# Performance work log

Hardware: AMD Instinct MI355X
Metric: run time of the kernel (lower is better)

## Reference

```python
import jax, jax.numpy as jnp
import numpy as np
from jax import lax


def setup_inputs() -> dict:
    key = jax.random.key(0)
    ks = jax.random.split(key, 6)
    T, B, I, H, K = 128, 64, 1024, 1024, 8
    s = 1.0 / np.sqrt(H)  # PyTorch LSTM init scale
    return {
        "x": jax.random.normal(ks[0], (T, B, I), dtype=jnp.float32),
        "coef": jax.random.uniform(ks[1], (T, K), dtype=jnp.float32),
        "w_ih": jax.random.uniform(ks[2], (K, 4 * H, I), dtype=jnp.float32, minval=-s, maxval=s),
        "w_hh": jax.random.uniform(ks[3], (K, 4 * H, H), dtype=jnp.float32, minval=-s, maxval=s),
        "b_ih": jax.random.uniform(ks[4], (K, 4 * H), dtype=jnp.float32, minval=-s, maxval=s),
        "b_hh": jax.random.uniform(ks[5], (K, 4 * H), dtype=jnp.float32, minval=-s, maxval=s),
        "h0": jnp.zeros((B, H), dtype=jnp.float32),
        "c0": jnp.zeros((B, H), dtype=jnp.float32),
    }


def reference(x, coef, w_ih, w_hh, b_ih, b_hh, h0, c0):
    # x: [T, B, I]; coef: [T, K]; w_ih: [K, 4H, I]; w_hh: [K, 4H, H]
    H = h0.shape[-1]
    cw = jax.nn.softmax(coef, axis=1)  # [T, K] mixture weights per timestep

    def step(carry, inp):
        h, c = carry            # [B, H], [B, H]
        xt, ct = inp            # [B, I], [K]
        # Synthesize this timestep's LSTM weights (mixture over k meta models)
        Wih = jnp.einsum('k,kgi->gi', ct, w_ih)   # [4H, I]
        Whh = jnp.einsum('k,kgh->gh', ct, w_hh)   # [4H, H]
        b = ct @ b_ih + ct @ b_hh                 # [4H]
        gates = xt @ Wih.T + h @ Whh.T + b        # [B, 4H]
        i, f, g, o = jnp.split(gates, 4, axis=-1)  # PyTorch gate order i,f,g,o
        i, f, o = jax.nn.sigmoid(i), jax.nn.sigmoid(f), jax.nn.sigmoid(o)
        g = jnp.tanh(g)
        c_new = f * c + i * g
        h_new = o * jnp.tanh(c_new)
        return (h_new, c_new), h_new

    (_, _), ys = lax.scan(step, (h0, c0), (x, cw))
    return ys  # [T, B, H] concatenated per-step outputs
```

## Files before the change

### kernel.cpp

```cpp
#include <hip/hip_runtime.h>
#include <math.h>
#include <stdint.h>

#define TT 128
#define BB 64
#define II 1024
#define HH 1024
#define KK 8
#define G4 4096
#define MM 8192
#define TCH 32
#define NCH (TT / TCH)

typedef _Float16 f16x8 __attribute__((ext_vector_type(8)));
typedef float    f32x4 __attribute__((ext_vector_type(4)));

#define OFF_CW    0
#define OFF_BIAS  4096
#define OFF_C     2101248
#define OFF_H0    2363392
#define OFF_H1    2494464
#define OFF_GX    2625536
#define OFF_WIH   69734400
#define OFF_X8    203952128
#define OFF_WCH   OFF_WIH
#define WS_REQ    338169856

__global__ __launch_bounds__(256) void softmax_bias_kernel(
    const float* __restrict__ coef,
    const float* __restrict__ b_ih,
    const float* __restrict__ b_hh,
    float* __restrict__ ws)
{
    int t = blockIdx.x;
    float c[KK];
    float m = -1e30f;
    #pragma unroll
    for (int k = 0; k < KK; ++k) { c[k] = coef[t*KK + k]; m = fmaxf(m, c[k]); }
    float s = 0.f;
    #pragma unroll
    for (int k = 0; k < KK; ++k) { c[k] = expf(c[k] - m); s += c[k]; }
    float inv = 1.f / s;
    #pragma unroll
    for (int k = 0; k < KK; ++k) c[k] *= inv;
    if (threadIdx.x < KK) ws[t*KK + threadIdx.x] = c[threadIdx.x];
    float* bias = ws + 1024;
    for (int g = threadIdx.x; g < G4; g += blockDim.x) {
        float acc = 0.f;
        #pragma unroll
        for (int k = 0; k < KK; ++k)
            acc += c[k] * (b_ih[k*G4 + g] + b_hh[k*G4 + g]);
        bias[t*G4 + g] = acc;
    }
}

__global__ __launch_bounds__(256) void conv_f16_kernel(
    const float* __restrict__ src, _Float16* __restrict__ dst, long n8)
{
    long v = (long)blockIdx.x * 256 + threadIdx.x;
    if (v >= n8) return;
    const float* s = src + v * 8;
    f16x8 o;
    #pragma unroll
    for (int e = 0; e < 8; ++e) o[e] = (_Float16)s[e];
    *(f16x8*)(dst + v * 8) = o;
}

__global__ __launch_bounds__(256) void mix_chunk_kernel(
    const float* __restrict__ w_hh,
    const float* __restrict__ cw,
    _Float16* __restrict__ wchunk,
    int t0)
{
    __shared__ float cws[TCH * KK];
    const int tid = threadIdx.x;
    if (tid < TCH * KK) cws[tid] = cw[t0 * KK + tid];

    long v = (long)blockIdx.x * 256 + tid;
    const int l  = (int)(v & 63);
    const int kk = (int)((v >> 6) & 31);
    const int bj = (int)(v >> 11);
    const int q  = l & 15;
    const int grow = (q >> 2) * HH + bj * 4 + (q & 3);
    const int col  = kk * 32 + 8 * (l >> 4);

    float w8[KK][8];
    #pragma unroll
    for (int k = 0; k < KK; ++k) {
        const float* s = w_hh + ((size_t)k * G4 + grow) * II + col;
        #pragma unroll
        for (int e = 0; e < 8; ++e) w8[k][e] = s[e];
    }
    __syncthreads();

    const size_t slot = ((size_t)bj * 32 + kk) * 64 + l;
    #pragma unroll 4
    for (int tt = 0; tt < TCH; ++tt) {
        float acc[8] = {0,0,0,0,0,0,0,0};
        #pragma unroll
        for (int k = 0; k < KK; ++k) {
            float c = cws[tt * KK + k];
            #pragma unroll
            for (int e = 0; e < 8; ++e) acc[e] += c * w8[k][e];
        }
        f16x8 o;
        #pragma unroll
        for (int e = 0; e < 8; ++e) o[e] = (_Float16)acc[e];
        *(f16x8*)(wchunk + ((size_t)tt << 22) + slot * 8) = o;
    }
}

__global__ __launch_bounds__(256) void x8_kernel(
    const float* __restrict__ x, const float* __restrict__ cw,
    _Float16* __restrict__ x8)
{
    long v = (long)blockIdx.x * 256 + threadIdx.x;
    if (v >= (long)KK * MM * (II/8)) return;
    int k   = (int)(v / (MM * (II/8)));
    long rem = v % (MM * (II/8));
    int row = (int)(rem / (II/8));
    int i8  = (int)(rem % (II/8));
    int t   = row >> 6;
    float sc = cw[t*KK + k];
    const float* s = x + (long)row * II + i8 * 8;
    f16x8 o;
    #pragma unroll
    for (int e = 0; e < 8; ++e) o[e] = (_Float16)(sc * s[e]);
    *(f16x8*)(x8 + v * 8) = o;
}

__global__ __launch_bounds__(256) void hinit_kernel(
    const float* __restrict__ h0, _Float16* __restrict__ hws)
{
    int idx = blockIdx.x * 256 + threadIdx.x;
    hws[idx] = (_Float16)h0[idx];
}

#define PAD 80
__global__ __launch_bounds__(256) void phaseA_gemm(
    const _Float16* __restrict__ x8,
    const _Float16* __restrict__ wih,
    _Float16* __restrict__ gx)
{
    __shared__ _Float16 As[128][PAD];
    __shared__ _Float16 Bs[128][PAD];
    const int tid  = threadIdx.x;
    const int lane = tid & 63;
    const int wv   = tid >> 6;
    const int wr   = wv >> 1, wc = wv & 1;
    const int bm   = blockIdx.x & 63;
    const int bn   = blockIdx.x >> 6;
    const size_t m0 = (size_t)bm * 128, n0 = (size_t)bn * 128;

    f32x4 acc[4][4];
    #pragma unroll
    for (int i = 0; i < 4; ++i)
        #pragma unroll
        for (int j = 0; j < 4; ++j) acc[i][j] = (f32x4){0.f,0.f,0.f,0.f};

    const int srow = tid >> 3;
    const int scol = (tid & 7) * 8;

    for (int kt = 0; kt < 128; ++kt) {
        const int kseg = kt >> 4;
        const int i0   = (kt & 15) * 64;
        const size_t abase = (size_t)kseg * MM * II + i0;
        const size_t bbase = (size_t)kseg * G4 * II + i0;
        #pragma unroll
        for (int it = 0; it < 4; ++it) {
            int r = it * 32 + srow;
            *(f16x8*)&As[r][scol] = *(const f16x8*)(x8 + abase + (m0 + r) * II + scol);
            *(f16x8*)&Bs[r][scol] = *(const f16x8*)(wih + bbase + (n0 + r) * II + scol);
        }
        __syncthreads();
        #pragma unroll
        for (int half = 0; half < 2; ++half) {
            const int kc = half * 32 + 8 * (lane >> 4);
            f16x8 a[4], b[4];
            #pragma unroll
            for (int mf = 0; mf < 4; ++mf)
                a[mf] = *(const f16x8*)&As[wr*64 + mf*16 + (lane & 15)][kc];
            #pragma unroll
            for (int nf = 0; nf < 4; ++nf)
                b[nf] = *(const f16x8*)&Bs[wc*64 + nf*16 + (lane & 15)][kc];
            #pragma unroll
            for (int mf = 0; mf < 4; ++mf)
                #pragma unroll
                for (int nf = 0; nf < 4; ++nf)
                    acc[mf][nf] = __builtin_amdgcn_mfma_f32_16x16x32_f16(
                        a[mf], b[nf], acc[mf][nf], 0, 0, 0);
        }
        __syncthreads();
    }
    #pragma unroll
    for (int mf = 0; mf < 4; ++mf)
        #pragma unroll
        for (int nf = 0; nf < 4; ++nf) {
            size_t col = n0 + wc*64 + nf*16 + (lane & 15);
            size_t rw  = m0 + wr*64 + mf*16 + 4*(lane >> 4);
            #pragma unroll
            for (int r = 0; r < 4; ++r)
                gx[(rw + r) * G4 + col] = (_Float16)acc[mf][nf][r];
        }
}

__global__ __launch_bounds__(512) void stepB5_kernel(
    const _Float16* __restrict__ wmix_t,
    const _Float16* __restrict__ gx_t,
    const float* __restrict__ bias_t,
    const _Float16* __restrict__ hin,
    _Float16* __restrict__ hout,
    float* __restrict__ cst,
    float* __restrict__ out_t)
{
    __shared__ float gpart[8][BB][17];

    const int tid  = threadIdx.x;
    const int lane = tid & 63;
    const int wv   = tid >> 6;
    const int bj   = blockIdx.x;
    const int j0   = bj * 4;
    const int q    = lane & 15;
    const int kch  = 8 * (lane >> 4);

    float pre_gx[4], pre_bias[4], pre_c = 0.f;
    const int eb  = tid & 63;
    const int ejj = tid >> 6;
    if (tid < 256) {
        #pragma unroll
        for (int gate = 0; gate < 4; ++gate) {
            pre_gx[gate]   = (float)gx_t[(size_t)eb * G4 + gate * HH + j0 + ejj];
            pre_bias[gate] = bias_t[gate * HH + j0 + ejj];
        }
        pre_c = cst[(size_t)eb * HH + j0 + ejj];
    }

    const _Float16* w0 = wmix_t + (((size_t)bj * 32 + 4 * wv) * 64) * 8;
    f16x8 pb[4];
    #pragma unroll
    for (int u = 0; u < 4; ++u)
        pb[u] = *(const f16x8*)(w0 + ((size_t)u * 64 + lane) * 8);

    f32x4 acc[4];
    #pragma unroll
    for (int mf = 0; mf < 4; ++mf) acc[mf] = (f32x4){0.f,0.f,0.f,0.f};

    #pragma unroll
    for (int u = 0; u < 4; ++u) {
        const int kk = 4 * wv + u;
        const int hp = kk * 32 + kch;
        f16x8 a[4];
        #pragma unroll
        for (int mf = 0; mf < 4; ++mf)
            a[mf] = *(const f16x8*)(hin + (size_t)(mf * 16 + q) * HH + hp);
        #pragma unroll
        for (int mf = 0; mf < 4; ++mf)
            acc[mf] = __builtin_amdgcn_mfma_f32_16x16x32_f16(a[mf], pb[u], acc[mf], 0, 0, 0);
    }

    #pragma unroll
    for (int mf = 0; mf < 4; ++mf) {
        #pragma unroll
        for (int r = 0; r < 4; ++r) {
            int m = mf * 16 + 4 * (lane >> 4) + r;
            gpart[wv][m][q] = acc[mf][r];
        }
    }
    __syncthreads();

    if (tid < 256) {
        const int j = j0 + ejj;
        float gval[4];
        #pragma unroll
        for (int gate = 0; gate < 4; ++gate) {
            int qq = gate * 4 + ejj;
            float v = 0.f;
            #pragma unroll
            for (int w = 0; w < 8; ++w) v += gpart[w][eb][qq];
            gval[gate] = v + pre_gx[gate] + pre_bias[gate];
        }
        float iv = 1.f / (1.f + expf(-gval[0]));
        float fv = 1.f / (1.f + expf(-gval[1]));
        float gv = tanhf(gval[2]);
        float ov = 1.f / (1.f + expf(-gval[3]));
        float c  = fv * pre_c + iv * gv;
        cst[(size_t)eb * HH + j] = c;
        float h  = ov * tanhf(c);
        out_t[(size_t)eb * HH + j] = h;
        hout[(size_t)eb * HH + j] = (_Float16)h;
    }
}

#define TI 128
__global__ __launch_bounds__(256) void step_kernel(
    const float* __restrict__ x_t, const float* __restrict__ hprev,
    const float* __restrict__ cprev, const float* __restrict__ w_ih,
    const float* __restrict__ w_hh, const float* __restrict__ cw_t,
    const float* __restrict__ bias_t, float* __restrict__ cstate,
    float* __restrict__ out_t)
{
    __shared__ float xh_s[BB][TI + 1];
    __shared__ float w_s[16][TI + 1];
    __shared__ float gex[4 * BB * 4];
    const int tid = threadIdx.x;
    const int j0 = blockIdx.x * 4;
    const int b = tid & 63;
    const int gate = tid >> 6;
    float cw[KK];
    #pragma unroll
    for (int k = 0; k < KK; ++k) cw[k] = cw_t[k];
    float acc[4] = {0.f, 0.f, 0.f, 0.f};
    for (int ci = 0; ci < II + HH; ci += TI) {
        for (int e = tid; e < BB * TI; e += 256) {
            int bb = e >> 7, cc = e & (TI - 1);
            int c = ci + cc;
            xh_s[bb][cc] = (c < II) ? x_t[bb * II + c] : hprev[bb * HH + (c - II)];
        }
        const float* wbase = (ci < II) ? w_ih : w_hh;
        const int cbase = (ci < II) ? ci : (ci - II);
        for (int e = tid; e < 16 * TI; e += 256) {
            int r = e >> 7, cc = e & (TI - 1);
            int grw = (r >> 2) * HH + j0 + (r & 3);
            size_t off = (size_t)grw * II + (size_t)(cbase + cc);
            float wm = 0.f;
            #pragma unroll
            for (int k = 0; k < KK; ++k)
                wm += cw[k] * wbase[(size_t)k * ((size_t)G4 * II) + off];
            w_s[r][cc] = wm;
        }
        __syncthreads();
        for (int c = 0; c < TI; ++c) {
            float xv = xh_s[b][c];
            #pragma unroll
            for (int d = 0; d < 4; ++d)
                acc[d] += xv * w_s[(gate << 2) + d][c];
        }
        __syncthreads();
    }
    #pragma unroll
    for (int d = 0; d < 4; ++d) {
        acc[d] += bias_t[gate * HH + j0 + d];
        gex[gate * 256 + b * 4 + d] = acc[d];
    }
    __syncthreads();
    const int b2 = tid & 63, d2 = tid >> 6;
    float iv = gex[0 * 256 + b2 * 4 + d2];
    float fv = gex[1 * 256 + b2 * 4 + d2];
    float gv = gex[2 * 256 + b2 * 4 + d2];
    float ov = gex[3 * 256 + b2 * 4 + d2];
    float si = 1.f / (1.f + expf(-iv));
    float sf = 1.f / (1.f + expf(-fv));
    float so = 1.f / (1.f + expf(-ov));
    float tg = tanhf(gv);
    int j = j0 + d2;
    float cold = cprev[b2 * HH + j];
    float cnew = sf * cold + si * tg;
    cstate[b2 * HH + j] = cnew;
    out_t[b2 * HH + j] = so * tanhf(cnew);
}

extern "C" void kernel_launch(void* const* d_in, const int* in_sizes, int n_in,
                              void* d_out, int out_size, void* d_ws, size_t ws_size,
                              hipStream_t stream) {
    const float* x    = (const float*)d_in[0];
    const float* coef = (const float*)d_in[1];
    const float* w_ih = (const float*)d_in[2];
    const float* w_hh = (const float*)d_in[3];
    const float* b_ih = (const float*)d_in[4];
    const float* b_hh = (const float*)d_in[5];
    const float* h0   = (const float*)d_in[6];
    const float* c0   = (const float*)d_in[7];
    float* out = (float*)d_out;
    char* ws   = (char*)d_ws;
    float* cw_f   = (float*)(ws + OFF_CW);
    float* bias_f = (float*)(ws + OFF_BIAS);
    float* c_f    = (float*)(ws + OFF_C);

    softmax_bias_kernel<<<TT, 256, 0, stream>>>(coef, b_ih, b_hh, (float*)ws);

    if (ws_size >= (size_t)WS_REQ) {
        _Float16* h0p  = (_Float16*)(ws + OFF_H0);
        _Float16* h1p  = (_Float16*)(ws + OFF_H1);
        _Float16* gx   = (_Float16*)(ws + OFF_GX);
        _Float16* wihf = (_Float16*)(ws + OFF_WIH);
        _Float16* x8   = (_Float16*)(ws + OFF_X8);
        _Float16* wch  = (_Float16*)(ws + OFF_WCH);

        conv_f16_kernel<<<16384, 256, 0, stream>>>(w_ih, wihf, (long)KK*G4*II/8);
        x8_kernel<<<32768, 256, 0, stream>>>(x, cw_f, x8);
        hinit_kernel<<<256, 256, 0, stream>>>(h0, h0p);
        hipMemcpyAsync(c_f, c0, (size_t)BB*HH*4, hipMemcpyDeviceToDevice, stream);

        phaseA_gemm<<<2048, 256, 0, stream>>>(x8, wihf, gx);

        for (int ch = 0; ch < NCH; ++ch) {
            const int t0 = ch * TCH;
            mix_chunk_kernel<<<2048, 256, 0, stream>>>(w_hh, cw_f, wch, t0);
            for (int tt = 0; tt < TCH; ++tt) {
                const int t = t0 + tt;
                stepB5_kernel<<<256, 512, 0, stream>>>(
                    wch + ((size_t)tt << 22),
                    gx + (size_t)t * BB * G4,
                    bias_f + (size_t)t * G4,
                    (t & 1) ? h1p : h0p,
                    (t & 1) ? h0p : h1p,
                    c_f,
                    out + (size_t)t * BB * HH);
            }
        }
    } else {
        for (int t = 0; t < TT; ++t) {
            const float* xt    = x + (size_t)t * BB * II;
            const float* hprev = (t == 0) ? h0 : out + (size_t)(t - 1) * BB * HH;
            const float* cprev = (t == 0) ? c0 : c_f;
            step_kernel<<<HH / 4, 256, 0, stream>>>(
                xt, hprev, cprev, w_ih, w_hh,
                cw_f + (size_t)t * KK,
                bias_f + (size_t)t * G4,
                c_f,
                out + (size_t)t * BB * HH);
        }
    }
}
```

Measured before the change: 2.360 ms.

## Replace input-projection mega-GEMM with per-timestep mixed-weight GEMMs

Instead of scaling x by each mixture coefficient and running one large GEMM with a reduction over K*I, this mixes w_ih into per-timestep f16 weights in chunks and runs a small 64x4096x1024 MFMA GEMM per timestep. That cuts input-projection FLOPs by about a factor of K and drops the x8 and w_ih conversion passes. In exchange it adds heavy memory traffic to write and re-read a mixed weight matrix for every timestep. The chunk size drops to 16, which doubles the number of mix launches for both w_ih and w_hh.

```diff
diff --git a/kernel.cpp b/kernel.cpp
--- a/kernel.cpp
+++ b/kernel.cpp
@@ -9,7 +9,7 @@
 #define KK 8
 #define G4 4096
 #define MM 8192
-#define TCH 32
+#define TCH 16
 #define NCH (TT / TCH)
 
 typedef _Float16 f16x8 __attribute__((ext_vector_type(8)));
@@ -21,9 +21,8 @@
 #define OFF_H0    2363392
 #define OFF_H1    2494464
 #define OFF_GX    2625536
-#define OFF_WIH   69734400
-#define OFF_X8    203952128
-#define OFF_WCH   OFF_WIH
+#define OFF_XF    69734400
+#define OFF_WCH   86511616
 #define WS_REQ    338169856
 
 __global__ __launch_bounds__(256) void softmax_bias_kernel(
@@ -67,7 +66,7 @@
 }
 
 __global__ __launch_bounds__(256) void mix_chunk_kernel(
-    const float* __restrict__ w_hh,
+    const float* __restrict__ wsrc,
     const float* __restrict__ cw,
     _Float16* __restrict__ wchunk,
     int t0)
@@ -87,7 +86,7 @@
     float w8[KK][8];
     #pragma unroll
     for (int k = 0; k < KK; ++k) {
-        const float* s = w_hh + ((size_t)k * G4 + grow) * II + col;
+        const float* s = wsrc + ((size_t)k * G4 + grow) * II + col;
         #pragma unroll
         for (int e = 0; e < 8; ++e) w8[k][e] = s[e];
     }
@@ -110,25 +109,6 @@
     }
 }
 
-__global__ __launch_bounds__(256) void x8_kernel(
-    const float* __restrict__ x, const float* __restrict__ cw,
-    _Float16* __restrict__ x8)
-{
-    long v = (long)blockIdx.x * 256 + threadIdx.x;
-    if (v >= (long)KK * MM * (II/8)) return;
-    int k   = (int)(v / (MM * (II/8)));
-    long rem = v % (MM * (II/8));
-    int row = (int)(rem / (II/8));
-    int i8  = (int)(rem % (II/8));
-    int t   = row >> 6;
-    float sc = cw[t*KK + k];
-    const float* s = x + (long)row * II + i8 * 8;
-    f16x8 o;
-    #pragma unroll
-    for (int e = 0; e < 8; ++e) o[e] = (_Float16)(sc * s[e]);
-    *(f16x8*)(x8 + v * 8) = o;
-}
-
 __global__ __launch_bounds__(256) void hinit_kernel(
     const float* __restrict__ h0, _Float16* __restrict__ hws)
 {
@@ -136,72 +116,74 @@
     hws[idx] = (_Float16)h0[idx];
 }
 
-#define PAD 80
-__global__ __launch_bounds__(256) void phaseA_gemm(
-    const _Float16* __restrict__ x8,
-    const _Float16* __restrict__ wih,
-    _Float16* __restrict__ gx)
-{
-    __shared__ _Float16 As[128][PAD];
-    __shared__ _Float16 Bs[128][PAD];
+__global__ __launch_bounds__(512) void gxA_kernel(
+    const _Float16* __restrict__ xf,
+    const _Float16* __restrict__ wch,
+    _Float16* __restrict__ gx,
+    int t0)
+{
+    __shared__ float gpart[8][BB][17];
+
     const int tid  = threadIdx.x;
     const int lane = tid & 63;
     const int wv   = tid >> 6;
-    const int wr   = wv >> 1, wc = wv & 1;
-    const int bm   = blockIdx.x & 63;
-    const int bn   = blockIdx.x >> 6;
-    const size_t m0 = (size_t)bm * 128, n0 = (size_t)bn * 128;
-
-    f32x4 acc[4][4];
-    #pragma unroll
-    for (int i = 0; i < 4; ++i)
-        #pragma unroll
-        for (int j = 0; j < 4; ++j) acc[i][j] = (f32x4){0.f,0.f,0.f,0.f};
-
-    const int srow = tid >> 3;
-    const int scol = (tid & 7) * 8;
-
-    for (int kt = 0; kt < 128; ++kt) {
-        const int kseg = kt >> 4;
-        const int i0   = (kt & 15) * 64;
-        const size_t abase = (size_t)kseg * MM * II + i0;
-        const size_t bbase = (size_t)kseg * G4 * II + i0;
-        #pragma unroll
-        for (int it = 0; it < 4; ++it) {
-            int r = it * 32 + srow;
-            *(f16x8*)&As[r][scol] = *(const f16x8*)(x8 + abase + (m0 + r) * II + scol);
-            *(f16x8*)&Bs[r][scol] = *(const f16x8*)(wih + bbase + (n0 + r) * II + scol);
-        }
-        __syncthreads();
-        #pragma unroll
-        for (int half = 0; half < 2; ++half) {
-            const int kc = half * 32 + 8 * (lane >> 4);
-            f16x8 a[4], b[4];
+    const int bj   = blockIdx.x & 255;
+    const int tt   = blockIdx.x >> 8;
+    const int t    = t0 + tt;
+    const int j0   = bj * 4;
+    const int q    = lane & 15;
+    const int kch  = 8 * (lane >> 4);
+
+    const _Float16* xf_t = xf + (size_t)t * BB * II;
+    _Float16*       gx_t = gx + (size_t)t * BB * G4;
+
+    const _Float16* w0 = wch + ((size_t)tt << 22)
+                             + (((size_t)bj * 32 + 4 * wv) * 64) * 8;
+    f16x8 pb[4];
+    #pragma unroll
+    for (int u = 0; u < 4; ++u)
+        pb[u] = *(const f16x8*)(w0 + ((size_t)u * 64 + lane) * 8);
+
+    f32x4 acc[4];
+    #pragma unroll
+    for (int mf = 0; mf < 4; ++mf) acc[mf] = (f32x4){0.f,0.f,0.f,0.f};
+
+    #pragma unroll
+    for (int u = 0; u < 4; ++u) {
+        const int kk = 4 * wv + u;
+        const int hp = kk * 32 + kch;
+        f16x8 a[4];
+        #pragma unroll
+        for (int mf = 0; mf < 4; ++mf)
+            a[mf] = *(const f16x8*)(xf_t + (size_t)(mf * 16 + q) * II + hp);
+        #pragma unroll
+        for (int mf = 0; mf < 4; ++mf)
+            acc[mf] = __builtin_amdgcn_mfma_f32_16x16x32_f16(a[mf], pb[u], acc[mf], 0, 0, 0);
+    }
+
+    #pragma unroll
+    for (int mf = 0; mf < 4; ++mf) {
+        #pragma unroll
+        for (int r = 0; r < 4; ++r) {
+            int m = mf * 16 + 4 * (lane >> 4) + r;
+            gpart[wv][m][q] = acc[mf][r];
+        }
+    }
+    __syncthreads();
+
+    if (tid < 256) {
+        const int b  = tid & 63;
+        const int jj = tid >> 6;
+        const int j  = j0 + jj;
+        #pragma unroll
+        for (int gate = 0; gate < 4; ++gate) {
+            int qq = gate * 4 + jj;
+            float v = 0.f;
             #pragma unroll
-            for (int mf = 0; mf < 4; ++mf)
-                a[mf] = *(const f16x8*)&As[wr*64 + mf*16 + (lane & 15)][kc];
-            #pragma unroll
-            for (int nf = 0; nf < 4; ++nf)
-                b[nf] = *(const f16x8*)&Bs[wc*64 + nf*16 + (lane & 15)][kc];
-            #pragma unroll
-            for (int mf = 0; mf < 4; ++mf)
-                #pragma unroll
-                for (int nf = 0; nf < 4; ++nf)
-                    acc[mf][nf] = __builtin_amdgcn_mfma_f32_16x16x32_f16(
-                        a[mf], b[nf], acc[mf][nf], 0, 0, 0);
-        }
-        __syncthreads();
-    }
-    #pragma unroll
-    for (int mf = 0; mf < 4; ++mf)
-        #pragma unroll
-        for (int nf = 0; nf < 4; ++nf) {
-            size_t col = n0 + wc*64 + nf*16 + (lane & 15);
-            size_t rw  = m0 + wr*64 + mf*16 + 4*(lane >> 4);
-            #pragma unroll
-            for (int r = 0; r < 4; ++r)
-                gx[(rw + r) * G4 + col] = (_Float16)acc[mf][nf][r];
-        }
+            for (int w = 0; w < 8; ++w) v += gpart[w][b][qq];
+            gx_t[(size_t)b * G4 + gate * HH + j] = (_Float16)v;
+        }
+    }
 }
 
 __global__ __launch_bounds__(512) void stepB5_kernel(
@@ -379,19 +361,21 @@
     softmax_bias_kernel<<<TT, 256, 0, stream>>>(coef, b_ih, b_hh, (float*)ws);
 
     if (ws_size >= (size_t)WS_REQ) {
-        _Float16* h0p  = (_Float16*)(ws + OFF_H0);
-        _Float16* h1p  = (_Float16*)(ws + OFF_H1);
-        _Float16* gx   = (_Float16*)(ws + OFF_GX);
-        _Float16* wihf = (_Float16*)(ws + OFF_WIH);
-        _Float16* x8   = (_Float16*)(ws + OFF_X8);
-        _Float16* wch  = (_Float16*)(ws + OFF_WCH);
-
-        conv_f16_kernel<<<16384, 256, 0, stream>>>(w_ih, wihf, (long)KK*G4*II/8);
-        x8_kernel<<<32768, 256, 0, stream>>>(x, cw_f, x8);
+        _Float16* h0p = (_Float16*)(ws + OFF_H0);
+        _Float16* h1p = (_Float16*)(ws + OFF_H1);
+        _Float16* gx  = (_Float16*)(ws + OFF_GX);
+        _Float16* xf  = (_Float16*)(ws + OFF_XF);
+        _Float16* wch = (_Float16*)(ws + OFF_WCH);
+
+        conv_f16_kernel<<<4096, 256, 0, stream>>>(x, xf, (long)MM * II / 8);
         hinit_kernel<<<256, 256, 0, stream>>>(h0, h0p);
         hipMemcpyAsync(c_f, c0, (size_t)BB*HH*4, hipMemcpyDeviceToDevice, stream);
 
-        phaseA_gemm<<<2048, 256, 0, stream>>>(x8, wihf, gx);
+        for (int ch = 0; ch < NCH; ++ch) {
+            const int t0 = ch * TCH;
+            mix_chunk_kernel<<<2048, 256, 0, stream>>>(w_ih, cw_f, wch, t0);
+            gxA_kernel<<<TCH * 256, 512, 0, stream>>>(xf, wch, gx, t0);
+        }
 
         for (int ch = 0; ch < NCH; ++ch) {
             const int t0 = ch * TCH;
```

Result: slower. 2.807 ms (+18.9%).

## Fold mixture coefficients into input GEMM epilogue instead of replicating scaled x

Applied to the files above, without the earlier changes.

Removes the kernel that materialized eight coefficient-scaled fp16 copies of x. The GEMM now reads a single fp16 copy of x and accumulates each meta-model segment into a partial accumulator, which is scaled by that timestep's coefficient and added to a total. This drops a large intermediate buffer write and read, at the cost of doubling the accumulator registers, which may reduce occupancy.

```diff
diff --git a/kernel.cpp b/kernel.cpp
--- a/kernel.cpp
+++ b/kernel.cpp
@@ -22,7 +22,7 @@
 #define OFF_H1    2494464
 #define OFF_GX    2625536
 #define OFF_WIH   69734400
-#define OFF_X8    203952128
+#define OFF_XF    203952128
 #define OFF_WCH   OFF_WIH
 #define WS_REQ    338169856
 
@@ -110,25 +110,6 @@
     }
 }
 
-__global__ __launch_bounds__(256) void x8_kernel(
-    const float* __restrict__ x, const float* __restrict__ cw,
-    _Float16* __restrict__ x8)
-{
-    long v = (long)blockIdx.x * 256 + threadIdx.x;
-    if (v >= (long)KK * MM * (II/8)) return;
-    int k   = (int)(v / (MM * (II/8)));
-    long rem = v % (MM * (II/8));
-    int row = (int)(rem / (II/8));
-    int i8  = (int)(rem % (II/8));
-    int t   = row >> 6;
-    float sc = cw[t*KK + k];
-    const float* s = x + (long)row * II + i8 * 8;
-    f16x8 o;
-    #pragma unroll
-    for (int e = 0; e < 8; ++e) o[e] = (_Float16)(sc * s[e]);
-    *(f16x8*)(x8 + v * 8) = o;
-}
-
 __global__ __launch_bounds__(256) void hinit_kernel(
     const float* __restrict__ h0, _Float16* __restrict__ hws)
 {
@@ -137,9 +118,10 @@
 }
 
 #define PAD 80
-__global__ __launch_bounds__(256) void phaseA_gemm(
-    const _Float16* __restrict__ x8,
+__global__ __launch_bounds__(256) void phaseA2_gemm(
+    const _Float16* __restrict__ xf,
     const _Float16* __restrict__ wih,
+    const float* __restrict__ cw,
     _Float16* __restrict__ gx)
 {
     __shared__ _Float16 As[128][PAD];
@@ -152,11 +134,19 @@
     const int bn   = blockIdx.x >> 6;
     const size_t m0 = (size_t)bm * 128, n0 = (size_t)bn * 128;
 
-    f32x4 acc[4][4];
+    const int t_wave = bm * 2 + wr;
+    float sc[KK];
+    #pragma unroll
+    for (int k = 0; k < KK; ++k) sc[k] = cw[t_wave * KK + k];
+
+    f32x4 accT[4][4], accP[4][4];
     #pragma unroll
     for (int i = 0; i < 4; ++i)
         #pragma unroll
-        for (int j = 0; j < 4; ++j) acc[i][j] = (f32x4){0.f,0.f,0.f,0.f};
+        for (int j = 0; j < 4; ++j) {
+            accT[i][j] = (f32x4){0.f,0.f,0.f,0.f};
+            accP[i][j] = (f32x4){0.f,0.f,0.f,0.f};
+        }
 
     const int srow = tid >> 3;
     const int scol = (tid & 7) * 8;
@@ -164,12 +154,11 @@
     for (int kt = 0; kt < 128; ++kt) {
         const int kseg = kt >> 4;
         const int i0   = (kt & 15) * 64;
-        const size_t abase = (size_t)kseg * MM * II + i0;
         const size_t bbase = (size_t)kseg * G4 * II + i0;
         #pragma unroll
         for (int it = 0; it < 4; ++it) {
             int r = it * 32 + srow;
-            *(f16x8*)&As[r][scol] = *(const f16x8*)(x8 + abase + (m0 + r) * II + scol);
+            *(f16x8*)&As[r][scol] = *(const f16x8*)(xf + (m0 + r) * II + i0 + scol);
             *(f16x8*)&Bs[r][scol] = *(const f16x8*)(wih + bbase + (n0 + r) * II + scol);
         }
         __syncthreads();
@@ -187,10 +176,22 @@
             for (int mf = 0; mf < 4; ++mf)
                 #pragma unroll
                 for (int nf = 0; nf < 4; ++nf)
-                    acc[mf][nf] = __builtin_amdgcn_mfma_f32_16x16x32_f16(
-                        a[mf], b[nf], acc[mf][nf], 0, 0, 0);
+                    accP[mf][nf] = __builtin_amdgcn_mfma_f32_16x16x32_f16(
+                        a[mf], b[nf], accP[mf][nf], 0, 0, 0);
         }
         __syncthreads();
+        if ((kt & 15) == 15) {
+            const float s = sc[kseg];
+            #pragma unroll
+            for (int mf = 0; mf < 4; ++mf)
+                #pragma unroll
+                for (int nf = 0; nf < 4; ++nf) {
+                    #pragma unroll
+                    for (int r = 0; r < 4; ++r)
+                        accT[mf][nf][r] += s * accP[mf][nf][r];
+                    accP[mf][nf] = (f32x4){0.f,0.f,0.f,0.f};
+                }
+        }
     }
     #pragma unroll
     for (int mf = 0; mf < 4; ++mf)
@@ -200,7 +201,7 @@
             size_t rw  = m0 + wr*64 + mf*16 + 4*(lane >> 4);
             #pragma unroll
             for (int r = 0; r < 4; ++r)
-                gx[(rw + r) * G4 + col] = (_Float16)acc[mf][nf][r];
+                gx[(rw + r) * G4 + col] = (_Float16)accT[mf][nf][r];
         }
 }
 
@@ -383,15 +384,15 @@
         _Float16* h1p  = (_Float16*)(ws + OFF_H1);
         _Float16* gx   = (_Float16*)(ws + OFF_GX);
         _Float16* wihf = (_Float16*)(ws + OFF_WIH);
-        _Float16* x8   = (_Float16*)(ws + OFF_X8);
+        _Float16* xf   = (_Float16*)(ws + OFF_XF);
         _Float16* wch  = (_Float16*)(ws + OFF_WCH);
 
         conv_f16_kernel<<<16384, 256, 0, stream>>>(w_ih, wihf, (long)KK*G4*II/8);
-        x8_kernel<<<32768, 256, 0, stream>>>(x, cw_f, x8);
+        conv_f16_kernel<<<4096, 256, 0, stream>>>(x, xf, (long)MM*II/8);
         hinit_kernel<<<256, 256, 0, stream>>>(h0, h0p);
         hipMemcpyAsync(c_f, c0, (size_t)BB*HH*4, hipMemcpyDeviceToDevice, stream);
 
-        phaseA_gemm<<<2048, 256, 0, stream>>>(x8, wihf, gx);
+        phaseA2_gemm<<<2048, 256, 0, stream>>>(xf, wihf, cw_f, gx);
 
         for (int ch = 0; ch < NCH; ++ch) {
             const int t0 = ch * TCH;
```

New measurement: 2.288 ms. -3.0%, faster.

## Rewrite input-projection GEMM with 256x256 tiles, async LDS loads and double buffering

Applied to the files above, without the earlier changes.

Replaces the 128x128 phase-A GEMM, which used synchronous register-staged loads, with a 256x256-tile, 512-thread kernel. The new kernel uses global_load_lds direct-to-LDS copies into double buffers with an XOR swizzle, fine-grained vmcnt waits, and s_setprio around MFMA bursts so loads for the next K tiles overlap compute. The aim is to hide memory latency and raise operand reuse in the large x·W_ih GEMM. The cost is heavy register pressure from 32 accumulators per lane, fewer blocks, and fragile hand-counted waitcnt ordering.

```diff
diff --git a/kernel.cpp b/kernel.cpp
--- a/kernel.cpp
+++ b/kernel.cpp
@@ -11,6 +11,7 @@
 #define MM 8192
 #define TCH 32
 #define NCH (TT / TCH)
+#define NT 128
 
 typedef _Float16 f16x8 __attribute__((ext_vector_type(8)));
 typedef float    f32x4 __attribute__((ext_vector_type(4)));
@@ -26,6 +27,10 @@
 #define OFF_WCH   OFF_WIH
 #define WS_REQ    338169856
 
+#define BARRIER() do { asm volatile("" ::: "memory"); \
+                       __builtin_amdgcn_s_barrier();  \
+                       asm volatile("" ::: "memory"); } while (0)
+
 __global__ __launch_bounds__(256) void softmax_bias_kernel(
     const float* __restrict__ coef,
     const float* __restrict__ b_ih,
@@ -64,50 +69,6 @@
     #pragma unroll
     for (int e = 0; e < 8; ++e) o[e] = (_Float16)s[e];
     *(f16x8*)(dst + v * 8) = o;
-}
-
-__global__ __launch_bounds__(256) void mix_chunk_kernel(
-    const float* __restrict__ w_hh,
-    const float* __restrict__ cw,
-    _Float16* __restrict__ wchunk,
-    int t0)
-{
-    __shared__ float cws[TCH * KK];
-    const int tid = threadIdx.x;
-    if (tid < TCH * KK) cws[tid] = cw[t0 * KK + tid];
-
-    long v = (long)blockIdx.x * 256 + tid;
-    const int l  = (int)(v & 63);
-    const int kk = (int)((v >> 6) & 31);
-    const int bj = (int)(v >> 11);
-    const int q  = l & 15;
-    const int grow = (q >> 2) * HH + bj * 4 + (q & 3);
-    const int col  = kk * 32 + 8 * (l >> 4);
-
-    float w8[KK][8];
-    #pragma unroll
-    for (int k = 0; k < KK; ++k) {
-        const float* s = w_hh + ((size_t)k * G4 + grow) * II + col;
-        #pragma unroll
-        for (int e = 0; e < 8; ++e) w8[k][e] = s[e];
-    }
-    __syncthreads();
-
-    const size_t slot = ((size_t)bj * 32 + kk) * 64 + l;
-    #pragma unroll 4
-    for (int tt = 0; tt < TCH; ++tt) {
-        float acc[8] = {0,0,0,0,0,0,0,0};
-        #pragma unroll
-        for (int k = 0; k < KK; ++k) {
-            float c = cws[tt * KK + k];
-            #pragma unroll
-            for (int e = 0; e < 8; ++e) acc[e] += c * w8[k][e];
-        }
-        f16x8 o;
-        #pragma unroll
-        for (int e = 0; e < 8; ++e) o[e] = (_Float16)acc[e];
-        *(f16x8*)(wchunk + ((size_t)tt << 22) + slot * 8) = o;
-    }
 }
 
 __global__ __launch_bounds__(256) void x8_kernel(
@@ -129,6 +90,50 @@
     *(f16x8*)(x8 + v * 8) = o;
 }
 
+__global__ __launch_bounds__(256) void mix_chunk_kernel(
+    const float* __restrict__ w_hh,
+    const float* __restrict__ cw,
+    _Float16* __restrict__ wchunk,
+    int t0)
+{
+    __shared__ float cws[TCH * KK];
+    const int tid = threadIdx.x;
+    if (tid < TCH * KK) cws[tid] = cw[t0 * KK + tid];
+
+    long v = (long)blockIdx.x * 256 + tid;
+    const int l  = (int)(v & 63);
+    const int kk = (int)((v >> 6) & 31);
+    const int bj = (int)(v >> 11);
+    const int q  = l & 15;
+    const int grow = (q >> 2) * HH + bj * 4 + (q & 3);
+    const int col  = kk * 32 + 8 * (l >> 4);
+
+    float w8[KK][8];
+    #pragma unroll
+    for (int k = 0; k < KK; ++k) {
+        const float* s = w_hh + ((size_t)k * G4 + grow) * II + col;
+        #pragma unroll
+        for (int e = 0; e < 8; ++e) w8[k][e] = s[e];
+    }
+    __syncthreads();
+
+    const size_t slot = ((size_t)bj * 32 + kk) * 64 + l;
+    #pragma unroll 4
+    for (int tt = 0; tt < TCH; ++tt) {
+        float acc[8] = {0,0,0,0,0,0,0,0};
+        #pragma unroll
+        for (int k = 0; k < KK; ++k) {
+            float c = cws[tt * KK + k];
+            #pragma unroll
+            for (int e = 0; e < 8; ++e) acc[e] += c * w8[k][e];
+        }
+        f16x8 o;
+        #pragma unroll
+        for (int e = 0; e < 8; ++e) o[e] = (_Float16)acc[e];
+        *(f16x8*)(wchunk + ((size_t)tt << 22) + slot * 8) = o;
+    }
+}
+
 __global__ __launch_bounds__(256) void hinit_kernel(
     const float* __restrict__ h0, _Float16* __restrict__ hws)
 {
@@ -136,68 +141,151 @@
     hws[idx] = (_Float16)h0[idx];
 }
 
-#define PAD 80
-__global__ __launch_bounds__(256) void phaseA_gemm(
+__device__ __forceinline__ int swz(int b) {
+    return b ^ (((b >> 9) & 1) << 5) ^ (((b >> 10) & 1) << 4);
+}
+
+__global__ __launch_bounds__(512) void phaseA3_gemm(
     const _Float16* __restrict__ x8,
     const _Float16* __restrict__ wih,
     _Float16* __restrict__ gx)
 {
-    __shared__ _Float16 As[128][PAD];
-    __shared__ _Float16 Bs[128][PAD];
+    __shared__ _Float16 ldsA[2 * 16384];
+    __shared__ _Float16 ldsB[2 * 16384];
+
     const int tid  = threadIdx.x;
     const int lane = tid & 63;
     const int wv   = tid >> 6;
-    const int wr   = wv >> 1, wc = wv & 1;
-    const int bm   = blockIdx.x & 63;
-    const int bn   = blockIdx.x >> 6;
-    const size_t m0 = (size_t)bm * 128, n0 = (size_t)bn * 128;
-
-    f32x4 acc[4][4];
-    #pragma unroll
-    for (int i = 0; i < 4; ++i)
+    const int wm   = wv >> 2;
+    const int wn   = wv & 3;
+    const int bm   = blockIdx.x & 31;
+    const int bn   = blockIdx.x >> 5;
+    const size_t m0 = (size_t)bm * 256, n0 = (size_t)bn * 256;
+
+    int srow[4], scol[4], pl2[4];
+    #pragma unroll
+    for (int j = 0; j < 4; ++j) {
+        int p = j * 8192 + tid * 16;
+        int L = swz(p);
+        srow[j] = L >> 7;
+        scol[j] = (L & 127) >> 1;
+        pl2[j]  = p >> 1;
+    }
+
+    auto stA = [&](int j, int tk) {
+        const int kseg = tk >> 4, i0v = (tk & 15) * 64;
+        const _Float16* s = x8 + (size_t)kseg * MM * II
+                               + (m0 + srow[j]) * II + i0v + scol[j];
+        __builtin_amdgcn_global_load_lds(s, &ldsA[(tk & 1) * 16384 + pl2[j]], 16, 0, 0);
+    };
+    auto stB = [&](int j, int tk) {
+        const int kseg = tk >> 4, i0v = (tk & 15) * 64;
+        const _Float16* s = wih + (size_t)kseg * G4 * II
+                               + (n0 + srow[j]) * II + i0v + scol[j];
+        __builtin_amdgcn_global_load_lds(s, &ldsB[(tk & 1) * 16384 + pl2[j]], 16, 0, 0);
+    };
+
+    const int baseA = (wm * 128 + (lane & 15)) * 128 + (lane >> 4) * 16;
+    const int baseB = (wn * 64  + (lane & 15)) * 128 + (lane >> 4) * 16;
+
+    auto rdA = [&](int buf, int mf, int ks) -> f16x8 {
+        int q = baseA + mf * 2048 + ks * 64;
+        return *(const f16x8*)((const char*)&ldsA[buf * 16384] + swz(q));
+    };
+    auto rdB = [&](int buf, int nf, int ks) -> f16x8 {
+        int q = baseB + nf * 2048 + ks * 64;
+        return *(const f16x8*)((const char*)&ldsB[buf * 16384] + swz(q));
+    };
+
+    f32x4 acc[8][4];
+    #pragma unroll
+    for (int i = 0; i < 8; ++i)
         #pragma unroll
         for (int j = 0; j < 4; ++j) acc[i][j] = (f32x4){0.f,0.f,0.f,0.f};
 
-    const int srow = tid >> 3;
-    const int scol = (tid & 7) * 8;
-
-    for (int kt = 0; kt < 128; ++kt) {
-        const int kseg = kt >> 4;
-        const int i0   = (kt & 15) * 64;
-        const size_t abase = (size_t)kseg * MM * II + i0;
-        const size_t bbase = (size_t)kseg * G4 * II + i0;
-        #pragma unroll
-        for (int it = 0; it < 4; ++it) {
-            int r = it * 32 + srow;
-            *(f16x8*)&As[r][scol] = *(const f16x8*)(x8 + abase + (m0 + r) * II + scol);
-            *(f16x8*)&Bs[r][scol] = *(const f16x8*)(wih + bbase + (n0 + r) * II + scol);
-        }
-        __syncthreads();
-        #pragma unroll
-        for (int half = 0; half < 2; ++half) {
-            const int kc = half * 32 + 8 * (lane >> 4);
-            f16x8 a[4], b[4];
-            #pragma unroll
-            for (int mf = 0; mf < 4; ++mf)
-                a[mf] = *(const f16x8*)&As[wr*64 + mf*16 + (lane & 15)][kc];
-            #pragma unroll
-            for (int nf = 0; nf < 4; ++nf)
-                b[nf] = *(const f16x8*)&Bs[wc*64 + nf*16 + (lane & 15)][kc];
-            #pragma unroll
-            for (int mf = 0; mf < 4; ++mf)
-                #pragma unroll
-                for (int nf = 0; nf < 4; ++nf)
-                    acc[mf][nf] = __builtin_amdgcn_mfma_f32_16x16x32_f16(
-                        a[mf], b[nf], acc[mf][nf], 0, 0, 0);
-        }
-        __syncthreads();
-    }
-    #pragma unroll
-    for (int mf = 0; mf < 4; ++mf)
+    stA(0,0); stA(2,0);
+    stB(0,0); stB(1,0);
+    stB(2,0); stB(3,0);
+    stA(1,0); stA(3,0);
+    stA(0,1); stA(2,1);
+    stB(0,1); stB(1,1);
+    stB(2,1); stB(3,1);
+
+    for (int kt = 0; kt < NT; ++kt) {
+        const int buf = kt & 1;
+        if (kt < NT - 1) { asm volatile("s_waitcnt vmcnt(8)" ::: "memory"); }
+        else             { asm volatile("s_waitcnt vmcnt(2)" ::: "memory"); }
+        BARRIER();
+        if (kt + 1 < NT) { stA(1, kt + 1); stA(3, kt + 1); }
+        f16x8 a0[4][2], b[4][2];
+        #pragma unroll
+        for (int mf = 0; mf < 4; ++mf) {
+            a0[mf][0] = rdA(buf, mf, 0);
+            a0[mf][1] = rdA(buf, mf, 1);
+        }
         #pragma unroll
         for (int nf = 0; nf < 4; ++nf) {
-            size_t col = n0 + wc*64 + nf*16 + (lane & 15);
-            size_t rw  = m0 + wr*64 + mf*16 + 4*(lane >> 4);
+            b[nf][0] = rdB(buf, nf, 0);
+            b[nf][1] = rdB(buf, nf, 1);
+        }
+        __builtin_amdgcn_s_setprio(1);
+        #pragma unroll
+        for (int mf = 0; mf < 4; ++mf)
+            #pragma unroll
+            for (int nf = 0; nf < 2; ++nf) {
+                acc[mf][nf] = __builtin_amdgcn_mfma_f32_16x16x32_f16(a0[mf][0], b[nf][0], acc[mf][nf], 0, 0, 0);
+                acc[mf][nf] = __builtin_amdgcn_mfma_f32_16x16x32_f16(a0[mf][1], b[nf][1], acc[mf][nf], 0, 0, 0);
+            }
+        __builtin_amdgcn_s_setprio(0);
+        BARRIER();
+        if (kt + 2 < NT) { stA(0, kt + 2); stA(2, kt + 2); }
+        __builtin_amdgcn_s_setprio(1);
+        #pragma unroll
+        for (int mf = 0; mf < 4; ++mf)
+            #pragma unroll
+            for (int nf = 2; nf < 4; ++nf) {
+                acc[mf][nf] = __builtin_amdgcn_mfma_f32_16x16x32_f16(a0[mf][0], b[nf][0], acc[mf][nf], 0, 0, 0);
+                acc[mf][nf] = __builtin_amdgcn_mfma_f32_16x16x32_f16(a0[mf][1], b[nf][1], acc[mf][nf], 0, 0, 0);
+            }
+        __builtin_amdgcn_s_setprio(0);
+        if (kt + 2 < NT)      { asm volatile("s_waitcnt vmcnt(10)" ::: "memory"); }
+        else if (kt + 1 < NT) { asm volatile("s_waitcnt vmcnt(8)"  ::: "memory"); }
+        else                  { asm volatile("s_waitcnt vmcnt(0)"  ::: "memory"); }
+        BARRIER();
+        if (kt + 2 < NT) { stB(0, kt + 2); stB(1, kt + 2); }
+        f16x8 a1[4][2];
+        #pragma unroll
+        for (int mf = 0; mf < 4; ++mf) {
+            a1[mf][0] = rdA(buf, mf + 4, 0);
+            a1[mf][1] = rdA(buf, mf + 4, 1);
+        }
+        __builtin_amdgcn_s_setprio(1);
+        #pragma unroll
+        for (int mf = 0; mf < 4; ++mf)
+            #pragma unroll
+            for (int nf = 2; nf < 4; ++nf) {
+                acc[mf+4][nf] = __builtin_amdgcn_mfma_f32_16x16x32_f16(a1[mf][0], b[nf][0], acc[mf+4][nf], 0, 0, 0);
+                acc[mf+4][nf] = __builtin_amdgcn_mfma_f32_16x16x32_f16(a1[mf][1], b[nf][1], acc[mf+4][nf], 0, 0, 0);
+            }
+        __builtin_amdgcn_s_setprio(0);
+        if (kt + 2 < NT) { stB(2, kt + 2); stB(3, kt + 2); }
+        __builtin_amdgcn_s_setprio(1);
+        #pragma unroll
+        for (int mf = 0; mf < 4; ++mf)
+            #pragma unroll
+            for (int nf = 0; nf < 2; ++nf) {
+                acc[mf+4][nf] = __builtin_amdgcn_mfma_f32_16x16x32_f16(a1[mf][0], b[nf][0], acc[mf+4][nf], 0, 0, 0);
+                acc[mf+4][nf] = __builtin_amdgcn_mfma_f32_16x16x32_f16(a1[mf][1], b[nf][1], acc[mf+4][nf], 0, 0, 0);
+            }
+        __builtin_amdgcn_s_setprio(0);
+    }
+
+    #pragma unroll
+    for (int mf = 0; mf < 8; ++mf)
+        #pragma unroll
+        for (int nf = 0; nf < 4; ++nf) {
+            size_t col = n0 + wn * 64 + nf * 16 + (lane & 15);
+            size_t rw  = m0 + wm * 128 + mf * 16 + 4 * (lane >> 4);
             #pragma unroll
             for (int r = 0; r < 4; ++r)
                 gx[(rw + r) * G4 + col] = (_Float16)acc[mf][nf][r];
@@ -391,7 +479,7 @@
         hinit_kernel<<<256, 256, 0, stream>>>(h0, h0p);
         hipMemcpyAsync(c_f, c0, (size_t)BB*HH*4, hipMemcpyDeviceToDevice, stream);
 
-        phaseA_gemm<<<2048, 256, 0, stream>>>(x8, wihf, gx);
+        phaseA3_gemm<<<512, 512, 0, stream>>>(x8, wihf, gx);
 
         for (int ch = 0; ch < NCH; ++ch) {
             const int t0 = ch * TCH;
```

Result: slower. 2.491 ms (+5.6%).
